# Optimization experiments

Hardware: AMD Instinct MI355X
Metric: run time of the kernel (lower is better)

The kernel has to match this reference:

```python
import jax, jax.numpy as jnp
import numpy as np

B, M, K = 32768, 8192, 16
EPS = 1e-5  # torch BatchNorm1d default


def _bn_relu(x, g, b):
    # training-mode batch norm (biased variance), matching torch BatchNorm1d forward
    m = x.mean(0)
    v = x.var(0)
    return jax.nn.relu(g * (x - m) * jax.lax.rsqrt(v + EPS) + b)


def _forward(pos, mc, mv, w1, b1, w2, b2, w3, b3, w4, b4, w5, b5, w6, b6,
             g1, be1, g2, be2, g3, be3, g4, be4, g5, be5, k):
    # squared pairwise distances [B, M]; same ordering as L2 norm used by torch.sort
    d2 = (pos * pos).sum(1, keepdims=True) + (mc * mc).sum(1)[None, :] - 2.0 * (pos @ mc.T)
    _, idx = jax.lax.top_k(-d2, k)                     # k nearest indices [B, k]
    nb = jnp.concatenate([mc[idx], mv[idx]], axis=-1)  # [B, k, 4] = (coord, value) per neighbor
    knn_feat = jnp.concatenate([pos, nb.reshape(pos.shape[0], k * 4)], axis=1)  # [B, 2+4k]
    x = _bn_relu(knn_feat @ w1 + b1, g1, be1)
    x = _bn_relu(x @ w2 + b2, g2, be2)
    x = _bn_relu(x @ w3 + b3, g3, be3)
    x = _bn_relu(x @ w4 + b4, g4, be4)
    x = _bn_relu(x @ w5 + b5, g5, be5)  # dropout = identity (eval mode)
    x = x @ w6 + b6
    return x, knn_feat


def setup_inputs() -> dict:
    key = jax.random.key(0)
    ks = jax.random.split(key, 32)
    d_in = 2 + K * 4
    dims = [(d_in, 128), (128, 256), (256, 512), (512, 128), (128, 64), (64, 2)]
    inp = {
        "pos": jax.random.normal(ks[0], (B, 2), jnp.float32),
        "measure_coords": jax.random.normal(ks[1], (M, 2), jnp.float32),
        "measure_vals": jax.random.normal(ks[2], (M, 2), jnp.float32),
    }
    for i, (fi, fo) in enumerate(dims, 1):
        inp[f"w{i}"] = jax.random.normal(ks[2 + 2 * i], (fi, fo), jnp.float32) / np.float32(np.sqrt(fi))
        inp[f"b{i}"] = jnp.zeros((fo,), jnp.float32)
    for i, n in enumerate([128, 256, 512, 128, 64], 1):
        inp[f"g{i}"] = jnp.ones((n,), jnp.float32)
        inp[f"be{i}"] = jnp.zeros((n,), jnp.float32)
    inp["k"] = K
    return inp


def reference(pos, measure_coords, measure_vals, w1, b1, w2, b2, w3, b3, w4, b4,
              w5, b5, w6, b6, g1, be1, g2, be2, g3, be3, g4, be4, g5, be5, k):
    return _forward(pos, measure_coords, measure_vals, w1, b1, w2, b2, w3, b3, w4,
                    b4, w5, b5, w6, b6, g1, be1, g2, be2, g3, be3, g4, be4, g5, be5, k)
```

## Files before the change

### kernel.cpp

```cpp
#include <hip/hip_runtime.h>

typedef unsigned short u16;
typedef unsigned int   u32;
typedef __attribute__((ext_vector_type(8))) short bf16x8;
typedef __attribute__((ext_vector_type(4))) float f32x4;

#define B_ROWS 32768
#define EPS_BN 1e-5f

__device__ __forceinline__ u16 f2bf(float f) {
  u32 u = __float_as_uint(f);
  u32 r = (u + 0x7FFFu + ((u >> 16) & 1u)) >> 16;
  return (u16)r;
}
__device__ __forceinline__ float bf2f(u16 h) {
  return __uint_as_float(((u32)h) << 16);
}

__device__ __forceinline__ float dcalc(float px, float py, float sp, float mx, float my) {
#pragma clang fp contract(off)
  float sm   = mx * mx + my * my;
  float pm   = px * mx;
  float dot  = __builtin_fmaf(py, my, pm);
  float spsm = sp + sm;
  return __builtin_fmaf(dot, -2.0f, spsm);
}
__device__ __forceinline__ float dcalc2(float px, float py, float sp, float mx, float my,
                                        float sm) {
#pragma clang fp contract(off)
  float pm   = px * mx;
  float dot  = __builtin_fmaf(py, my, pm);
  float spsm = sp + sm;
  return __builtin_fmaf(dot, -2.0f, spsm);
}
__device__ __forceinline__ float smcalc(float mx, float my) {
#pragma clang fp contract(off)
  return mx * mx + my * my;
}
__device__ __forceinline__ float spcalc(float px, float py) {
#pragma clang fp contract(off)
  return px * px + py * py;
}
#define MED3 __builtin_amdgcn_fmed3f

__global__ __launch_bounds__(256, 4)
void knn_kernel(const float2* __restrict__ pos, const float2* __restrict__ mc,
                const float2* __restrict__ mv, float* __restrict__ knn_out,
                u16* __restrict__ X0)
{
  __shared__ float tv[32 * 130];
  __shared__ float tstS[32];
  __shared__ float qxS[32], qyS[32], qsS[32];
  __shared__ unsigned long long qmaskS[32];
  __shared__ int   qcnt[32];
  __shared__ int   ntaskS;

  const int t = threadIdx.x;
  const int g = t >> 6;
  const int s = t & 63;
  const int q0 = blockIdx.x * 32;

  float px[8], py[8], sp[8];
#pragma unroll
  for (int j = 0; j < 8; ++j) {
    float2 p = pos[q0 + g * 8 + j];
    px[j] = p.x; py[j] = p.y; sp[j] = spcalc(p.x, p.y);
  }
#pragma unroll
  for (int j = 0; j < 8; ++j) {
    if (s == j) { qxS[g * 8 + j] = px[j]; qyS[g * 8 + j] = py[j]; qsS[g * 8 + j] = sp[j]; }
  }

  const float4* mc4 = (const float4*)mc;
  const int b4 = s * 64;

  float z0[8], z1[8];
#pragma unroll
  for (int j = 0; j < 8; ++j) { z0[j] = __builtin_inff(); z1[j] = __builtin_inff(); }

  float4 cur = mc4[b4];
  for (int i = 0; i < 64; ++i) {
    float4 nxt = mc4[b4 + ((i + 1) & 63)];
    float smA = smcalc(cur.x, cur.y);
    float smB = smcalc(cur.z, cur.w);
#pragma unroll
    for (int j = 0; j < 8; ++j) {
      float dA = dcalc2(px[j], py[j], sp[j], cur.x, cur.y, smA);
      z1[j] = MED3(z0[j], dA, z1[j]); z0[j] = fminf(z0[j], dA);
      float dB = dcalc2(px[j], py[j], sp[j], cur.z, cur.w, smB);
      z1[j] = MED3(z0[j], dB, z1[j]); z0[j] = fminf(z0[j], dB);
    }
    cur = nxt;
  }
#pragma unroll
  for (int j = 0; j < 8; ++j) {
    float2 zz; zz.x = z0[j]; zz.y = z1[j];
    *(float2*)(&tv[(g * 8 + j) * 130 + s * 2]) = zz;
  }
  __syncthreads();

  if (t < 32) {
    float ch[16];
#pragma unroll
    for (int j = 0; j < 16; ++j) ch[j] = __builtin_inff();
    for (int k = 0; k < 128; ++k) {
      float v = tv[t * 130 + k];
#pragma unroll
      for (int j = 15; j >= 1; --j) ch[j] = MED3(ch[j-1], v, ch[j]);
      ch[0] = fminf(ch[0], v);
    }
    tstS[t] = ch[15];
    qcnt[t] = 0;
    if (t == 0) ntaskS = 0;
  }
  __syncthreads();

  {
    float Tq[8];
#pragma unroll
    for (int j = 0; j < 8; ++j) Tq[j] = tstS[g * 8 + j];
    unsigned long long m;
#pragma unroll
    for (int j = 0; j < 8; ++j) {
      m = __ballot(z0[j] <= Tq[j]);
      if (s == j) qmaskS[g * 8 + j] = m;
    }
  }
  __syncthreads();

  u16* qcand = (u16*)tv;
  u16* taskS = ((u16*)tv) + 2048;
  if (t < 32) {
    unsigned long long m = qmaskS[t];
    int c = __popcll(m);
    int off = atomicAdd(&ntaskS, c);
    u16 qb = (u16)(t << 6);
    while (m) {
      int b = (int)__builtin_ctzll(m);
      m &= m - 1;
      taskS[off++] = qb | (u16)b;
    }
  }
  __syncthreads();

  const int ntask = ntaskS;
  for (int i0 = t; i0 < ntask; i0 += 256) {
    const int task = taskS[i0];
    const int qrow = task >> 6;
    const int sl   = task & 63;
    const float qx = qxS[qrow], qy = qyS[qrow];
    const float qs = qsS[qrow], qT = tstS[qrow];
    const float4* mbase = mc4 + sl * 64;
    const int bpt = sl * 128;
#pragma unroll 4
    for (int i = 0; i < 64; ++i) {
      float4 c2 = mbase[i];
      float smA = smcalc(c2.x, c2.y);
      float smB = smcalc(c2.z, c2.w);
      float dA = dcalc2(qx, qy, qs, c2.x, c2.y, smA);
      float dB = dcalc2(qx, qy, qs, c2.z, c2.w, smB);
      if (dA <= qT) {
        int o = atomicAdd(&qcnt[qrow], 1);
        if (o < 64) qcand[qrow * 64 + o] = (u16)(bpt + 2 * i);
      }
      if (dB <= qT) {
        int o = atomicAdd(&qcnt[qrow], 1);
        if (o < 64) qcand[qrow * 64 + o] = (u16)(bpt + 2 * i + 1);
      }
    }
  }
  __syncthreads();

  if (t < 32) {
    const int q = q0 + t;
    float2 p = pos[q];
    const float sq = spcalc(p.x, p.y);
    int cnt = qcnt[t]; if (cnt > 64) cnt = 64;
    float fd[16]; int fi[16];
#pragma unroll
    for (int j = 0; j < 16; ++j) { fd[j] = __builtin_inff(); fi[j] = 0x7fffffff; }
    for (int j = 0; j < cnt; ++j) {
      int ci = qcand[t * 64 + j];
      float2 m = mc[ci];
      float d = dcalc(p.x, p.y, sq, m.x, m.y);
      bool cc = (d < fd[15]) || (d == fd[15] && ci < fi[15]);
      if (cc) {
#pragma unroll
        for (int k = 15; k >= 1; --k) {
          bool cm = (d < fd[k-1]) || (d == fd[k-1] && ci < fi[k-1]);
          if (cc) {
            if (cm) { fd[k] = fd[k-1]; fi[k] = fi[k-1]; }
            else    { fd[k] = d;       fi[k] = ci;      }
          }
          cc = cm;
        }
        if (cc) { fd[0] = d; fi[0] = ci; }
      }
    }
    float* orow = knn_out + (size_t)q * 66;
    u16*   xrow = X0 + (size_t)q * 96;
    orow[0] = p.x; orow[1] = p.y;
    xrow[0] = f2bf(p.x); xrow[1] = f2bf(p.y);
#pragma unroll
    for (int j = 0; j < 16; ++j) {
      int ci = fi[j];
      float2 m = mc[ci], v = mv[ci];
      orow[2 + 4*j + 0] = m.x; orow[2 + 4*j + 1] = m.y;
      orow[2 + 4*j + 2] = v.x; orow[2 + 4*j + 3] = v.y;
      xrow[2 + 4*j + 0] = f2bf(m.x); xrow[2 + 4*j + 1] = f2bf(m.y);
      xrow[2 + 4*j + 2] = f2bf(v.x); xrow[2 + 4*j + 3] = f2bf(v.y);
    }
#pragma unroll
    for (int c = 66; c < 96; ++c) xrow[c] = 0;
  }
}

__global__ __launch_bounds__(256)
void prep_wt_all(const float* __restrict__ w1, const float* __restrict__ w2,
                 const float* __restrict__ w3, const float* __restrict__ w4,
                 const float* __restrict__ w5,
                 u16* __restrict__ wt1, u16* __restrict__ wt2, u16* __restrict__ wt3,
                 u16* __restrict__ wt4, u16* __restrict__ wt5)
{
  const int l = blockIdx.y;
  const float* w; u16* wt; int K, N, Kp;
  if (l == 0)      { w = w1; wt = wt1; K = 66;  N = 128; Kp = 96;  }
  else if (l == 1) { w = w2; wt = wt2; K = 128; N = 256; Kp = 128; }
  else if (l == 2) { w = w3; wt = wt3; K = 256; N = 512; Kp = 256; }
  else if (l == 3) { w = w4; wt = wt4; K = 512; N = 128; Kp = 512; }
  else             { w = w5; wt = wt5; K = 128; N = 64;  Kp = 128; }
  int i = blockIdx.x * 256 + threadIdx.x;
  if (i >= N * Kp) return;
  int n = i / Kp, kp = i - n * Kp;
  float v = (kp < K) ? w[(size_t)kp * N + n] : 0.0f;
  wt[i] = f2bf(v);
}

template<int BN, bool FUSE>
__global__ __launch_bounds__(256)
void gemm_bn_kernel(const u16* __restrict__ X, int Kw,
                    const u16* __restrict__ WT,
                    const float* __restrict__ bias,
                    const float* __restrict__ psum, const float* __restrict__ psq,
                    const float* __restrict__ gw,   const float* __restrict__ bw,
                    u16* __restrict__ Z, int N,
                    float* __restrict__ csum, float* __restrict__ csq)
{
  constexpr int BM = 128;
  constexpr int AST = 40;
  __shared__ u16 Ash[BM * AST];
  __shared__ u16 Bsh[BN * AST];
  __shared__ float redS[4][BN];
  __shared__ float redQ[4][BN];
  __shared__ float scA[512];
  __shared__ float ttA[512];

  const int t = threadIdx.x;
  const int wave = t >> 6;
  const int lane = t & 63;
  const int lr = lane & 15;
  const int qd = lane >> 4;
  const int m0 = blockIdx.x * BM;
  const int n0 = blockIdx.y * BN;

  if (FUSE) {
    const float invB = 1.0f / 32768.0f;
    for (int c = t; c < Kw; c += 256) {
      float mean = psum[c] * invB;
      float var  = __fmaf_rn(-mean, mean, psq[c] * invB);
      float sc   = gw[c] * rsqrtf(var + EPS_BN);
      scA[c] = sc;
      ttA[c] = __fmaf_rn(-mean, sc, bw[c]);
    }
    __syncthreads();
  }

  f32x4 acc[2][BN / 16];
#pragma unroll
  for (int a = 0; a < 2; ++a)
#pragma unroll
    for (int b = 0; b < BN / 16; ++b) {
      acc[a][b][0] = 0.f; acc[a][b][1] = 0.f; acc[a][b][2] = 0.f; acc[a][b][3] = 0.f;
    }

  const int sr = t >> 2;
  const int sk = (t & 3) * 8;

  for (int k0 = 0; k0 < Kw; k0 += 32) {
#pragma unroll
    for (int rr = 0; rr < 2; ++rr) {
      int r = sr + rr * 64;
      uint4 g = *(const uint4*)(&X[(size_t)(m0 + r) * Kw + k0 + sk]);
      if (FUSE) {
        u32 w[4] = {g.x, g.y, g.z, g.w};
        u32 o[4];
#pragma unroll
        for (int e = 0; e < 4; ++e) {
          int kk = k0 + sk + 2 * e;
          float lo = bf2f((u16)(w[e] & 0xffffu));
          float hi = bf2f((u16)(w[e] >> 16));
          float yl = fmaxf(__fmaf_rn(lo, scA[kk],     ttA[kk]),     0.0f);
          float yh = fmaxf(__fmaf_rn(hi, scA[kk + 1], ttA[kk + 1]), 0.0f);
          o[e] = (u32)f2bf(yl) | ((u32)f2bf(yh) << 16);
        }
        g.x = o[0]; g.y = o[1]; g.z = o[2]; g.w = o[3];
      }
      *(uint4*)(&Ash[r * AST + sk]) = g;
    }
    if (BN == 128) {
#pragma unroll
      for (int rr = 0; rr < 2; ++rr) {
        int n = sr + rr * 64;
        *(uint4*)(&Bsh[n * AST + sk]) =
            *(const uint4*)(&WT[(size_t)(n0 + n) * Kw + k0 + sk]);
      }
    } else {
      int n = sr;
      *(uint4*)(&Bsh[n * AST + sk]) =
          *(const uint4*)(&WT[(size_t)(n0 + n) * Kw + k0 + sk]);
    }
    __syncthreads();
    bf16x8 af0 = *(const bf16x8*)(&Ash[(wave * 32 + lr) * AST + qd * 8]);
    bf16x8 af1 = *(const bf16x8*)(&Ash[(wave * 32 + 16 + lr) * AST + qd * 8]);
#pragma unroll
    for (int ct = 0; ct < BN / 16; ++ct) {
      bf16x8 bfr = *(const bf16x8*)(&Bsh[(ct * 16 + lr) * AST + qd * 8]);
      acc[0][ct] = __builtin_amdgcn_mfma_f32_16x16x32_bf16(af0, bfr, acc[0][ct], 0, 0, 0);
      acc[1][ct] = __builtin_amdgcn_mfma_f32_16x16x32_bf16(af1, bfr, acc[1][ct], 0, 0, 0);
    }
    __syncthreads();
  }

#pragma unroll
  for (int ct = 0; ct < BN / 16; ++ct) {
    int cg = n0 + ct * 16 + lr;
    float bv = bias[cg];
    float s = 0.f, sqv = 0.f;
#pragma unroll
    for (int rt = 0; rt < 2; ++rt) {
#pragma unroll
      for (int r = 0; r < 4; ++r) {
        float z = acc[rt][ct][r] + bv;
        int row = m0 + wave * 32 + rt * 16 + qd * 4 + r;
        Z[(size_t)row * N + cg] = f2bf(z);
        s += z;
        sqv = __fmaf_rn(z, z, sqv);
      }
    }
    s   += __shfl_xor(s, 16);   s   += __shfl_xor(s, 32);
    sqv += __shfl_xor(sqv, 16); sqv += __shfl_xor(sqv, 32);
    if (qd == 0) { redS[wave][ct * 16 + lr] = s; redQ[wave][ct * 16 + lr] = sqv; }
  }
  __syncthreads();
  if (t < BN) {
    float s  = redS[0][t] + redS[1][t] + redS[2][t] + redS[3][t];
    float sv = redQ[0][t] + redQ[1][t] + redQ[2][t] + redQ[3][t];
    atomicAdd(&csum[n0 + t], s);
    atomicAdd(&csq[n0 + t], sv);
  }
}

__global__ __launch_bounds__(256)
void gemv6_kernel(const u16* __restrict__ Z5, const float* __restrict__ w6,
                  const float* __restrict__ b6,
                  const float* __restrict__ psum, const float* __restrict__ psq,
                  const float* __restrict__ gw,   const float* __restrict__ bw,
                  float* __restrict__ out)
{
  __shared__ float wsh[128];
  __shared__ float scs[64];
  __shared__ float tts[64];
  const int t = threadIdx.x;
  if (t < 128) wsh[t] = w6[t];
  if (t < 64) {
    const float invB = 1.0f / 32768.0f;
    float mean = psum[t] * invB;
    float var  = __fmaf_rn(-mean, mean, psq[t] * invB);
    float sc   = gw[t] * rsqrtf(var + EPS_BN);
    scs[t] = sc;
    tts[t] = __fmaf_rn(-mean, sc, bw[t]);
  }
  __syncthreads();
  const int q = blockIdx.x * 256 + t;
  const uint4* xv = (const uint4*)(Z5 + (size_t)q * 64);
  float a0 = 0.f, a1 = 0.f;
#pragma unroll
  for (int cc = 0; cc < 8; ++cc) {
    uint4 pk = xv[cc];
    u32 u[4] = {pk.x, pk.y, pk.z, pk.w};
#pragma unroll
    for (int uu = 0; uu < 4; ++uu) {
      int k = cc * 8 + uu * 2;
      float z0 = bf2f((u16)(u[uu] & 0xffffu));
      float z1 = bf2f((u16)(u[uu] >> 16));
      float x0 = fmaxf(__fmaf_rn(z0, scs[k],     tts[k]),     0.0f);
      float x1 = fmaxf(__fmaf_rn(z1, scs[k + 1], tts[k + 1]), 0.0f);
      x0 = bf2f(f2bf(x0));
      x1 = bf2f(f2bf(x1));
      a0 = __fmaf_rn(x0, wsh[2 * k + 0], a0);
      a1 = __fmaf_rn(x0, wsh[2 * k + 1], a1);
      a0 = __fmaf_rn(x1, wsh[2 * k + 2], a0);
      a1 = __fmaf_rn(x1, wsh[2 * k + 3], a1);
    }
  }
  float2 o; o.x = a0 + b6[0]; o.y = a1 + b6[1];
  ((float2*)out)[q] = o;
}

extern "C" void kernel_launch(void* const* d_in, const int* in_sizes, int n_in,
                              void* d_out, int out_size, void* d_ws, size_t ws_size,
                              hipStream_t stream)
{
  const float2* pos = (const float2*)d_in[0];
  const float2* mc  = (const float2*)d_in[1];
  const float2* mv  = (const float2*)d_in[2];
  const float* w1 = (const float*)d_in[3];  const float* b1 = (const float*)d_in[4];
  const float* w2 = (const float*)d_in[5];  const float* b2 = (const float*)d_in[6];
  const float* w3 = (const float*)d_in[7];  const float* b3 = (const float*)d_in[8];
  const float* w4 = (const float*)d_in[9];  const float* b4 = (const float*)d_in[10];
  const float* w5 = (const float*)d_in[11]; const float* b5 = (const float*)d_in[12];
  const float* w6 = (const float*)d_in[13]; const float* b6 = (const float*)d_in[14];
  const float* g1 = (const float*)d_in[15]; const float* be1 = (const float*)d_in[16];
  const float* g2 = (const float*)d_in[17]; const float* be2 = (const float*)d_in[18];
  const float* g3 = (const float*)d_in[19]; const float* be3 = (const float*)d_in[20];
  const float* g4 = (const float*)d_in[21]; const float* be4 = (const float*)d_in[22];
  const float* g5 = (const float*)d_in[23]; const float* be5 = (const float*)d_in[24];

  char* ws = (char*)d_ws;
  u16* X0   = (u16*)(ws + 0);
  u16* ZA   = (u16*)(ws + 6291456);
  u16* ZB   = (u16*)(ws + 39845888);
  u16* WT1  = (u16*)(ws + 73400320);
  u16* WT2  = (u16*)(ws + 73424896);
  u16* WT3  = (u16*)(ws + 73490432);
  u16* WT4  = (u16*)(ws + 73752576);
  u16* WT5  = (u16*)(ws + 73883648);
  float* stats = (float*)(ws + 73900032);
  float* s1 = stats;        float* s2 = stats + 128;  float* s3 = stats + 384;
  float* s4 = stats + 896;  float* s5 = stats + 1024;
  float* sqb = stats + 1088;
  float* q1 = sqb;          float* q2 = sqb + 128;    float* q3 = sqb + 384;
  float* q4 = sqb + 896;    float* q5 = sqb + 1024;

  float* outX = (float*)d_out;
  float* outK = outX + 2 * B_ROWS;

  hipMemsetAsync(stats, 0, 2176 * sizeof(float), stream);
  prep_wt_all<<<dim3(512, 5), 256, 0, stream>>>(w1, w2, w3, w4, w5, WT1, WT2, WT3, WT4, WT5);
  knn_kernel<<<dim3(1024), 256, 0, stream>>>(pos, mc, mv, outK, X0);

  gemm_bn_kernel<64, false><<<dim3(256, 2), 256, 0, stream>>>(
      X0, 96, WT1, b1, nullptr, nullptr, nullptr, nullptr, ZA, 128, s1, q1);
  gemm_bn_kernel<64, true><<<dim3(256, 4), 256, 0, stream>>>(
      ZA, 128, WT2, b2, s1, q1, g1, be1, ZB, 256, s2, q2);
  gemm_bn_kernel<64, true><<<dim3(256, 8), 256, 0, stream>>>(
      ZB, 256, WT3, b3, s2, q2, g2, be2, ZA, 512, s3, q3);
  gemm_bn_kernel<64, true><<<dim3(256, 2), 256, 0, stream>>>(
      ZA, 512, WT4, b4, s3, q3, g3, be3, ZB, 128, s4, q4);
  gemm_bn_kernel<64, true><<<dim3(256, 1), 256, 0, stream>>>(
      ZB, 128, WT5, b5, s4, q4, g4, be4, ZA, 64, s5, q5);
  gemv6_kernel<<<dim3(128), 256, 0, stream>>>(ZA, w6, b6, s5, q5, g5, be5, outX);

  (void)in_sizes; (void)n_in; (void)out_size; (void)ws_size;
}
```

Measured before the change: 342.2 us.

## Interleave measure-point slices for coalesced loads and vectorize kNN output stores

Changes the assignment of measure points to lanes so each lane handles a strided set of points (i*64+s) instead of a contiguous block. Consecutive lanes then load adjacent float4s, which coalesces the scan and refinement loads. Candidate index computation is updated to match. The output writes of knn_feat and the bf16 X0 row are also vectorized into float2 and packed u32 stores, with the zero padding written as u32 words.

Result: no change. 335.6 us (-1.9%).

```diff
diff --git a/kernel.cpp b/kernel.cpp
--- a/kernel.cpp
+++ b/kernel.cpp
@@ -12,6 +12,9 @@
   u32 u = __float_as_uint(f);
   u32 r = (u + 0x7FFFu + ((u >> 16) & 1u)) >> 16;
   return (u16)r;
+}
+__device__ __forceinline__ u32 pk2bf(float a, float b) {
+  return (u32)f2bf(a) | ((u32)f2bf(b) << 16);
 }
 __device__ __forceinline__ float bf2f(u16 h) {
   return __uint_as_float(((u32)h) << 16);
@@ -72,15 +75,14 @@
   }
 
   const float4* mc4 = (const float4*)mc;
-  const int b4 = s * 64;
 
   float z0[8], z1[8];
 #pragma unroll
   for (int j = 0; j < 8; ++j) { z0[j] = __builtin_inff(); z1[j] = __builtin_inff(); }
 
-  float4 cur = mc4[b4];
+  float4 cur = mc4[s];
   for (int i = 0; i < 64; ++i) {
-    float4 nxt = mc4[b4 + ((i + 1) & 63)];
+    float4 nxt = mc4[((i + 1) & 63) * 64 + s];
     float smA = smcalc(cur.x, cur.y);
     float smB = smcalc(cur.z, cur.w);
 #pragma unroll
@@ -150,22 +152,21 @@
     const int sl   = task & 63;
     const float qx = qxS[qrow], qy = qyS[qrow];
     const float qs = qsS[qrow], qT = tstS[qrow];
-    const float4* mbase = mc4 + sl * 64;
-    const int bpt = sl * 128;
 #pragma unroll 4
     for (int i = 0; i < 64; ++i) {
-      float4 c2 = mbase[i];
+      float4 c2 = mc4[i * 64 + sl];
+      const int pidx = 2 * (i * 64 + sl);
       float smA = smcalc(c2.x, c2.y);
       float smB = smcalc(c2.z, c2.w);
       float dA = dcalc2(qx, qy, qs, c2.x, c2.y, smA);
       float dB = dcalc2(qx, qy, qs, c2.z, c2.w, smB);
       if (dA <= qT) {
         int o = atomicAdd(&qcnt[qrow], 1);
-        if (o < 64) qcand[qrow * 64 + o] = (u16)(bpt + 2 * i);
+        if (o < 64) qcand[qrow * 64 + o] = (u16)pidx;
       }
       if (dB <= qT) {
         int o = atomicAdd(&qcnt[qrow], 1);
-        if (o < 64) qcand[qrow * 64 + o] = (u16)(bpt + 2 * i + 1);
+        if (o < 64) qcand[qrow * 64 + o] = (u16)(pidx + 1);
       }
     }
   }
@@ -199,19 +200,20 @@
     }
     float* orow = knn_out + (size_t)q * 66;
     u16*   xrow = X0 + (size_t)q * 96;
-    orow[0] = p.x; orow[1] = p.y;
-    xrow[0] = f2bf(p.x); xrow[1] = f2bf(p.y);
+    float2 pp; pp.x = p.x; pp.y = p.y;
+    *(float2*)(&orow[0]) = pp;
+    *(u32*)(&xrow[0]) = pk2bf(p.x, p.y);
 #pragma unroll
     for (int j = 0; j < 16; ++j) {
       int ci = fi[j];
       float2 m = mc[ci], v = mv[ci];
-      orow[2 + 4*j + 0] = m.x; orow[2 + 4*j + 1] = m.y;
-      orow[2 + 4*j + 2] = v.x; orow[2 + 4*j + 3] = v.y;
-      xrow[2 + 4*j + 0] = f2bf(m.x); xrow[2 + 4*j + 1] = f2bf(m.y);
-      xrow[2 + 4*j + 2] = f2bf(v.x); xrow[2 + 4*j + 3] = f2bf(v.y);
-    }
-#pragma unroll
-    for (int c = 66; c < 96; ++c) xrow[c] = 0;
+      *(float2*)(&orow[2 + 4*j]) = m;
+      *(float2*)(&orow[4 + 4*j]) = v;
+      *(u32*)(&xrow[2 + 4*j]) = pk2bf(m.x, m.y);
+      *(u32*)(&xrow[4 + 4*j]) = pk2bf(v.x, v.y);
+    }
+#pragma unroll
+    for (int c = 33; c < 48; ++c) ((u32*)xrow)[c] = 0;
   }
 }
 
```
